# Kernel tuning notes

Hardware: AMD Instinct MI355X
Metric: run time of the kernel (lower is better)

Reference implementation:

```python
import jax, jax.numpy as jnp
import numpy as np

DIM = 1024
HEADS = 16
SCALE = DIM ** (-0.5)  # NOTE: module scales by full dim, not head_dim


def setup_inputs() -> dict:
    key = jax.random.key(0)
    k1, k2, k3, k4 = jax.random.split(key, 4)
    x = jax.random.normal(k1, (4, 2048, DIM), dtype=jnp.float32)
    # torch Linear weights: y = x @ W.T
    w_qkv = jax.random.normal(k2, (3 * DIM, DIM), dtype=jnp.float32) * (DIM ** -0.5)
    w_out = jax.random.normal(k3, (DIM, DIM), dtype=jnp.float32) * (DIM ** -0.5)
    b_out = jax.random.normal(k4, (DIM,), dtype=jnp.float32) * 0.01
    return {"x": x, "w_qkv": w_qkv, "w_out": w_out, "b_out": b_out}


def reference(x, w_qkv, w_out, b_out):
    b, n, _ = x.shape
    h = HEADS
    d = DIM // h
    qkv = x @ w_qkv.T                                   # [b, n, 3*dim]
    qkv = qkv.reshape(b, n, 3, h, d)                    # split (qkv h d)
    qkv = jnp.transpose(qkv, (2, 0, 3, 1, 4))           # [3, b, h, n, d]
    q, k, v = qkv[0], qkv[1], qkv[2]
    dots = jnp.einsum('bhid,bhjd->bhij', q, k) * SCALE  # [b, h, n, n]
    attn = jax.nn.softmax(dots, axis=-1)
    out = jnp.einsum('bhij,bhjd->bhid', attn, v)        # [b, h, n, d]
    out = jnp.transpose(out, (0, 2, 1, 3)).reshape(b, n, h * d)
    return out @ w_out.T + b_out
```

## Files before the change

kernel.cpp:

```cpp
#include <hip/hip_runtime.h>

typedef short bf16x8 __attribute__((ext_vector_type(8)));
typedef float f32x4 __attribute__((ext_vector_type(4)));
typedef float f32x16 __attribute__((ext_vector_type(16)));

static __device__ __forceinline__ unsigned short f2bf(float f) {
  union { float f; unsigned u; } v; v.f = f;
  unsigned r = v.u + 0x7fffu + ((v.u >> 16) & 1u);
  return (unsigned short)(r >> 16);
}

static __device__ __forceinline__ unsigned pk2bf(float lo, float hi) {
  union { float f; unsigned u; } a, b; a.f = lo; b.f = hi;
  unsigned ra = a.u + 0x7fffu + ((a.u >> 16) & 1u);
  unsigned rb = b.u + 0x7fffu + ((b.u >> 16) & 1u);
  return __builtin_amdgcn_perm(rb, ra, 0x07060302);
}

static __device__ __forceinline__ void gll16(const unsigned short* g,
                                             unsigned short* l) {
  __builtin_amdgcn_global_load_lds(
      (const __attribute__((address_space(1))) unsigned int*)g,
      (__attribute__((address_space(3))) unsigned int*)l, 16, 0, 0);
}

__global__ void cvt_kernel(const float* __restrict__ src,
                           unsigned short* __restrict__ dst, int n4) {
  int i = blockIdx.x * blockDim.x + threadIdx.x;
  if (i >= n4) return;
  float4 f = ((const float4*)src)[i];
  ushort4 o;
  o.x = f2bf(f.x); o.y = f2bf(f.y); o.z = f2bf(f.z); o.w = f2bf(f.w);
  ((ushort4*)dst)[i] = o;
}

#define TM 128
#define TN 128
#define BK 64

template <int EPI>
__global__ __launch_bounds__(256, 2)
void gemm_bt(const unsigned short* __restrict__ X,
             const unsigned short* __restrict__ W,
             unsigned short* __restrict__ QKV, float* __restrict__ OUT,
             const float* __restrict__ bias, int M, int N, int K) {
  __shared__ __align__(16) unsigned short As[TM * BK];
  __shared__ __align__(16) unsigned short Bs[TN * BK];

  const int tid = threadIdx.x;
  const int lane = tid & 63;
  const int wave = tid >> 6;
  const int quad = lane >> 4;
  const int l16 = lane & 15;
  const int wm = wave >> 1, wn = wave & 1;
  const int rc = l16 & 7;

  const int m0 = blockIdx.y * TM;
  const int n0 = blockIdx.x * TN;

  const int sr = lane >> 3;
  const int gsc = ((lane & 7) ^ sr) * 8;

  f32x4 zero = {0.f, 0.f, 0.f, 0.f};
  f32x4 acc[4][4];
#pragma unroll
  for (int i = 0; i < 4; i++)
#pragma unroll
    for (int j = 0; j < 4; j++) acc[i][j] = zero;

  for (int k0 = 0; k0 < K; k0 += BK) {
    __syncthreads();
#pragma unroll
    for (int c = 0; c < 4; c++) {
      int row = wave * 32 + c * 8;
      gll16(&X[(size_t)(m0 + row + sr) * K + k0 + gsc], &As[row * BK]);
      gll16(&W[(size_t)(n0 + row + sr) * K + k0 + gsc], &Bs[row * BK]);
    }
    __syncthreads();
#pragma unroll
    for (int kk = 0; kk < 2; kk++) {
      bf16x8 af[4], bfr[4];
      const int csw = ((kk * 4 + quad) ^ rc) * 8;
#pragma unroll
      for (int t = 0; t < 4; t++) {
        af[t]  = *(const bf16x8*)&As[(wm * 64 + t * 16 + l16) * BK + csw];
        bfr[t] = *(const bf16x8*)&Bs[(wn * 64 + t * 16 + l16) * BK + csw];
      }
#pragma unroll
      for (int mt = 0; mt < 4; mt++)
#pragma unroll
        for (int nt = 0; nt < 4; nt++)
          acc[mt][nt] = __builtin_amdgcn_mfma_f32_16x16x32_bf16(
              af[mt], bfr[nt], acc[mt][nt], 0, 0, 0);
    }
  }

#pragma unroll
  for (int mt = 0; mt < 4; mt++) {
#pragma unroll
    for (int nt = 0; nt < 4; nt++) {
      if (EPI == 0) {
        int nbase = n0 + wn * 64 + nt * 16;
        int which = nbase >> 10;
        if (which == 2) {
          int rem = (nbase + l16) & 1023;
          int h = rem >> 6, dd = rem & 63;
          int growb = m0 + wm * 64 + mt * 16 + quad * 4;
          int b = growb >> 11, nn0 = growb & 2047;
          ushort4 o;
          o.x = f2bf(acc[mt][nt][0]);
          o.y = f2bf(acc[mt][nt][1]);
          o.z = f2bf(acc[mt][nt][2]);
          o.w = f2bf(acc[mt][nt][3]);
          *(ushort4*)&QKV[16777216u + (((size_t)(b * 16 + h) * 64 + dd) << 11) + nn0] = o;
        } else {
#pragma unroll
          for (int r = 0; r < 4; r++) {
            int grow = m0 + wm * 64 + mt * 16 + quad * 4 + r;
            int gcol = nbase + l16;
            int rem = gcol & 1023;
            int h = rem >> 6, dd = rem & 63;
            float v = acc[mt][nt][r];
            if (which == 0) v *= 0.04508422f;
            int b = grow >> 11, nn = grow & 2047;
            QKV[(size_t)which * 8388608 +
                ((size_t)(b * 16 + h) * 2048 + nn) * 64 + dd] = f2bf(v);
          }
        }
      } else {
#pragma unroll
        for (int r = 0; r < 4; r++) {
          int grow = m0 + wm * 64 + mt * 16 + quad * 4 + r;
          int gcol = n0 + wn * 64 + nt * 16 + l16;
          OUT[(size_t)grow * N + gcol] = acc[mt][nt][r] + bias[gcol];
        }
      }
    }
  }
}

__global__ __launch_bounds__(256, 4)
void attn_kernel(const unsigned short* __restrict__ Qg,
                 const unsigned short* __restrict__ Kg,
                 const unsigned short* __restrict__ Vg,
                 unsigned short* __restrict__ AO) {
  __shared__ __align__(16) unsigned short K_s[2][64 * 64];
  __shared__ __align__(16) unsigned short V_s[2][64 * 64];

  const int tid = threadIdx.x;
  const int lane = tid & 63;
  const int wave = tid >> 6;
  const int l31 = lane & 31;
  const int hh = lane >> 5;
  const int rc = l31 & 7;

  const int qb = blockIdx.x;
  const int bh = blockIdx.y;
  const size_t base = (size_t)bh * 131072;
  const int q0 = qb * 128 + wave * 32;

  bf16x8 bq[4];
#pragma unroll
  for (int ks = 0; ks < 4; ks++)
    bq[ks] = *(const bf16x8*)&Qg[base + (size_t)(q0 + l31) * 64 + ks * 16 + hh * 8];

  f32x16 O[2];
#pragma unroll
  for (int dt = 0; dt < 2; dt++)
#pragma unroll
    for (int r = 0; r < 16; r++) O[dt][r] = 0.f;
  float lrow = 0.f;

  const int sr = lane >> 3;
  const int gsc = ((lane & 7) ^ sr) * 8;
  const unsigned short* Kb = Kg + base;
  const unsigned short* Vb = Vg + base;

#define PREFETCH(J0, B)                                                    \
  {                                                                        \
    _Pragma("unroll") for (int c = 0; c < 2; c++) {                        \
      int r = wave * 16 + c * 8;                                           \
      gll16(&Kb[(size_t)((J0) + r + sr) * 64 + gsc], &K_s[B][r * 64]);     \
      gll16(&Vb[(size_t)(r + sr) * 2048 + (J0) + gsc], &V_s[B][r * 64]);   \
    }                                                                      \
  }

  PREFETCH(0, 0);

  for (int t = 0; t < 32; t++) {
    __syncthreads();
    if (t < 31) PREFETCH((t + 1) * 64, (t + 1) & 1);
    const unsigned short* Kc = K_s[t & 1];
    const unsigned short* Vc = V_s[t & 1];

    f32x16 S[2];
#pragma unroll
    for (int sub = 0; sub < 2; sub++) {
      f32x16 a;
#pragma unroll
      for (int r = 0; r < 16; r++) a[r] = 0.f;
#pragma unroll
      for (int ks = 0; ks < 4; ks++) {
        bf16x8 kf = *(const bf16x8*)&Kc[(sub * 32 + l31) * 64 +
                                        (((ks * 2 + hh) ^ rc) * 8)];
        a = __builtin_amdgcn_mfma_f32_32x32x16_bf16(kf, bq[ks], a, 0, 0, 0);
      }
      S[sub] = a;
    }

    float rsum = 0.f;
#pragma unroll
    for (int sub = 0; sub < 2; sub++)
#pragma unroll
      for (int r = 0; r < 16; r++) {
        float p = __builtin_amdgcn_exp2f(S[sub][r]);
        S[sub][r] = p;
        rsum += p;
      }
    lrow += rsum;

#pragma unroll
    for (int win = 0; win < 4; win++) {
      const int sub = win >> 1, kk = win & 1;
      const int g0 = kk * 2, g1 = kk * 2 + 1;
      unsigned a00 = pk2bf(S[sub][4 * g0 + 0], S[sub][4 * g0 + 1]);
      unsigned a01 = pk2bf(S[sub][4 * g0 + 2], S[sub][4 * g0 + 3]);
      unsigned a10 = pk2bf(S[sub][4 * g1 + 0], S[sub][4 * g1 + 1]);
      unsigned a11 = pk2bf(S[sub][4 * g1 + 2], S[sub][4 * g1 + 3]);
      unsigned b00 = __shfl_xor((int)a00, 32);
      unsigned b01 = __shfl_xor((int)a01, 32);
      unsigned b10 = __shfl_xor((int)a10, 32);
      unsigned b11 = __shfl_xor((int)a11, 32);
      union { unsigned u[4]; bf16x8 v; } fr;
      fr.u[0] = hh ? b10 : a00;
      fr.u[1] = hh ? b11 : a01;
      fr.u[2] = hh ? a10 : b00;
      fr.u[3] = hh ? a11 : b01;
      bf16x8 pf = fr.v;
#pragma unroll
      for (int dt = 0; dt < 2; dt++) {
        bf16x8 vf = *(const bf16x8*)&Vc[(dt * 32 + l31) * 64 +
                                        (((win * 2 + hh) ^ rc) * 8)];
        O[dt] = __builtin_amdgcn_mfma_f32_32x32x16_bf16(vf, pf, O[dt], 0, 0, 0);
      }
    }
  }

  const int b4 = bh >> 4, head = bh & 15;
  lrow += __shfl_xor(lrow, 32);
  float inv = 1.0f / lrow;
  int row = b4 * 2048 + q0 + l31;
#pragma unroll
  for (int dt = 0; dt < 2; dt++)
#pragma unroll
    for (int g = 0; g < 4; g++) {
      ushort4 o;
      o.x = f2bf(O[dt][4 * g + 0] * inv);
      o.y = f2bf(O[dt][4 * g + 1] * inv);
      o.z = f2bf(O[dt][4 * g + 2] * inv);
      o.w = f2bf(O[dt][4 * g + 3] * inv);
      *(ushort4*)&AO[(size_t)row * 1024 + head * 64 + dt * 32 + 8 * g + 4 * hh] = o;
    }
}

extern "C" void kernel_launch(void* const* d_in, const int* in_sizes, int n_in,
                              void* d_out, int out_size, void* d_ws,
                              size_t ws_size, hipStream_t stream) {
  const float* x     = (const float*)d_in[0];
  const float* w_qkv = (const float*)d_in[1];
  const float* w_out = (const float*)d_in[2];
  const float* b_out = (const float*)d_in[3];
  float* out = (float*)d_out;

  unsigned short* ws = (unsigned short*)d_ws;
  unsigned short* Xbf  = ws;
  unsigned short* Wqkv = ws + 8388608;
  unsigned short* Wout = ws + 11534336;
  unsigned short* QKV  = ws + 12582912;
  unsigned short* AO   = ws;

  cvt_kernel<<<8192, 256, 0, stream>>>(x, Xbf, 2097152);
  cvt_kernel<<<3072, 256, 0, stream>>>(w_qkv, Wqkv, 786432);
  cvt_kernel<<<1024, 256, 0, stream>>>(w_out, Wout, 262144);

  gemm_bt<0><<<dim3(3072 / TN, 8192 / TM), 256, 0, stream>>>(
      Xbf, Wqkv, QKV, nullptr, nullptr, 8192, 3072, 1024);

  attn_kernel<<<dim3(16, 64), 256, 0, stream>>>(
      QKV, QKV + 8388608, QKV + 16777216, AO);

  gemm_bt<1><<<dim3(1024 / TN, 8192 / TM), 256, 0, stream>>>(
      AO, Wout, nullptr, out, b_out, 8192, 1024, 1024);
}
```

Measured before the change: 278.7 us.

## Stage K/V tiles through registers into padded LDS and use permlane32 swap

Replaces the direct global-to-LDS async loads with register-staged prefetch: the next K/V tile is loaded into registers at the top of each iteration and written to the other LDS buffer after compute, with one barrier per iteration. The XOR swizzle is replaced by a padded row stride of 72 elements to avoid bank conflicts. The P-fragment lane exchange uses permlane32_swap when available instead of four shuffles and selects. This trades async LDS DMA for extra VGPRs and LDS space, which may pressure occupancy under the 4-blocks launch bound.

After: 273.8 us. No clear change (-1.7%).

```diff
diff --git a/kernel.cpp b/kernel.cpp
--- a/kernel.cpp
+++ b/kernel.cpp
@@ -3,6 +3,7 @@
 typedef short bf16x8 __attribute__((ext_vector_type(8)));
 typedef float f32x4 __attribute__((ext_vector_type(4)));
 typedef float f32x16 __attribute__((ext_vector_type(16)));
+typedef unsigned u32x2 __attribute__((ext_vector_type(2)));
 
 static __device__ __forceinline__ unsigned short f2bf(float f) {
   union { float f; unsigned u; } v; v.f = f;
@@ -139,20 +140,21 @@
   }
 }
 
+#define SK 72
+
 __global__ __launch_bounds__(256, 4)
 void attn_kernel(const unsigned short* __restrict__ Qg,
                  const unsigned short* __restrict__ Kg,
                  const unsigned short* __restrict__ Vg,
                  unsigned short* __restrict__ AO) {
-  __shared__ __align__(16) unsigned short K_s[2][64 * 64];
-  __shared__ __align__(16) unsigned short V_s[2][64 * 64];
+  __shared__ __align__(16) unsigned short K_s[2][64 * SK];
+  __shared__ __align__(16) unsigned short V_s[2][64 * SK];
 
   const int tid = threadIdx.x;
   const int lane = tid & 63;
   const int wave = tid >> 6;
   const int l31 = lane & 31;
   const int hh = lane >> 5;
-  const int rc = l31 & 7;
 
   const int qb = blockIdx.x;
   const int bh = blockIdx.y;
@@ -171,27 +173,27 @@
     for (int r = 0; r < 16; r++) O[dt][r] = 0.f;
   float lrow = 0.f;
 
-  const int sr = lane >> 3;
-  const int gsc = ((lane & 7) ^ sr) * 8;
-  const unsigned short* Kb = Kg + base;
-  const unsigned short* Vb = Vg + base;
-
-#define PREFETCH(J0, B)                                                    \
-  {                                                                        \
-    _Pragma("unroll") for (int c = 0; c < 2; c++) {                        \
-      int r = wave * 16 + c * 8;                                           \
-      gll16(&Kb[(size_t)((J0) + r + sr) * 64 + gsc], &K_s[B][r * 64]);     \
-      gll16(&Vb[(size_t)(r + sr) * 2048 + (J0) + gsc], &V_s[B][r * 64]);   \
-    }                                                                      \
-  }
-
-  PREFETCH(0, 0);
+  const int sr = lane >> 3, sc = (lane & 7) * 8;
+  const unsigned short* Kp = Kg + base + (size_t)(wave * 16 + sr) * 64 + sc;
+  const unsigned short* Vp = Vg + base + (size_t)(wave * 16 + sr) * 2048 + sc;
+  const int woff = (wave * 16 + sr) * SK + sc;
+
+  uint4 kr0, kr1, vr0, vr1;
+  kr0 = *(const uint4*)Kp;           kr1 = *(const uint4*)(Kp + 512);
+  vr0 = *(const uint4*)Vp;           vr1 = *(const uint4*)(Vp + 16384);
+  *(uint4*)&K_s[0][woff] = kr0;      *(uint4*)&K_s[0][woff + 8 * SK] = kr1;
+  *(uint4*)&V_s[0][woff] = vr0;      *(uint4*)&V_s[0][woff + 8 * SK] = vr1;
+  __syncthreads();
 
   for (int t = 0; t < 32; t++) {
-    __syncthreads();
-    if (t < 31) PREFETCH((t + 1) * 64, (t + 1) & 1);
     const unsigned short* Kc = K_s[t & 1];
     const unsigned short* Vc = V_s[t & 1];
+    if (t < 31) {
+      const unsigned short* kp = Kp + (size_t)(t + 1) * 4096;
+      const unsigned short* vp = Vp + (size_t)(t + 1) * 64;
+      kr0 = *(const uint4*)kp;  kr1 = *(const uint4*)(kp + 512);
+      vr0 = *(const uint4*)vp;  vr1 = *(const uint4*)(vp + 16384);
+    }
 
     f32x16 S[2];
 #pragma unroll
@@ -201,8 +203,7 @@
       for (int r = 0; r < 16; r++) a[r] = 0.f;
 #pragma unroll
       for (int ks = 0; ks < 4; ks++) {
-        bf16x8 kf = *(const bf16x8*)&Kc[(sub * 32 + l31) * 64 +
-                                        (((ks * 2 + hh) ^ rc) * 8)];
+        bf16x8 kf = *(const bf16x8*)&Kc[(sub * 32 + l31) * SK + ks * 16 + hh * 8];
         a = __builtin_amdgcn_mfma_f32_32x32x16_bf16(kf, bq[ks], a, 0, 0, 0);
       }
       S[sub] = a;
@@ -227,23 +228,35 @@
       unsigned a01 = pk2bf(S[sub][4 * g0 + 2], S[sub][4 * g0 + 3]);
       unsigned a10 = pk2bf(S[sub][4 * g1 + 0], S[sub][4 * g1 + 1]);
       unsigned a11 = pk2bf(S[sub][4 * g1 + 2], S[sub][4 * g1 + 3]);
+      union { unsigned u[4]; bf16x8 v; } fr;
+#if __has_builtin(__builtin_amdgcn_permlane32_swap)
+      u32x2 r0 = __builtin_amdgcn_permlane32_swap(a00, a10, false, false);
+      u32x2 r1 = __builtin_amdgcn_permlane32_swap(a01, a11, false, false);
+      fr.u[0] = r0.x; fr.u[1] = r1.x; fr.u[2] = r0.y; fr.u[3] = r1.y;
+#else
       unsigned b00 = __shfl_xor((int)a00, 32);
       unsigned b01 = __shfl_xor((int)a01, 32);
       unsigned b10 = __shfl_xor((int)a10, 32);
       unsigned b11 = __shfl_xor((int)a11, 32);
-      union { unsigned u[4]; bf16x8 v; } fr;
       fr.u[0] = hh ? b10 : a00;
       fr.u[1] = hh ? b11 : a01;
       fr.u[2] = hh ? a10 : b00;
       fr.u[3] = hh ? a11 : b01;
+#endif
       bf16x8 pf = fr.v;
 #pragma unroll
       for (int dt = 0; dt < 2; dt++) {
-        bf16x8 vf = *(const bf16x8*)&Vc[(dt * 32 + l31) * 64 +
-                                        (((win * 2 + hh) ^ rc) * 8)];
+        bf16x8 vf = *(const bf16x8*)&Vc[(dt * 32 + l31) * SK + win * 16 + hh * 8];
         O[dt] = __builtin_amdgcn_mfma_f32_32x32x16_bf16(vf, pf, O[dt], 0, 0, 0);
       }
     }
+
+    if (t < 31) {
+      const int nb = (t + 1) & 1;
+      *(uint4*)&K_s[nb][woff] = kr0;  *(uint4*)&K_s[nb][woff + 8 * SK] = kr1;
+      *(uint4*)&V_s[nb][woff] = vr0;  *(uint4*)&V_s[nb][woff + 8 * SK] = vr1;
+    }
+    __syncthreads();
   }
 
   const int b4 = bh >> 4, head = bh & 15;
```
